# Kernel tuning notes

Hardware: AMD Instinct MI355X
Metric: run time of the kernel (lower is better)

## Reference

```python
import jax, jax.numpy as jnp
import numpy as np

DIM = 1024
BLOCK = 64
N_BLOCKS = DIM // BLOCK
N = 65536
INIT_SCALE = 0.01


def setup_inputs() -> dict:
    key = jax.random.key(0)
    k1, k2 = jax.random.split(key)
    x = jax.random.normal(k1, (N, DIM), dtype=jnp.float32)
    skew_params = jax.random.normal(k2, (N_BLOCKS, BLOCK, BLOCK), dtype=jnp.float32) * INIT_SCALE
    perm = jnp.asarray(np.random.default_rng(0).permutation(DIM), dtype=jnp.int64)
    return {"x": x, "skew_params": skew_params, "perm": perm}


def reference(x, skew_params, perm):
    # Skew-symmetrize each block: A = P - P^T, shape [K, b, b]
    A = skew_params - jnp.swapaxes(skew_params, -1, -2)
    # Per-block orthogonal matrices via matrix exponential, [K, b, b]
    B = jax.vmap(jax.scipy.linalg.expm)(A)
    # Block-diagonal matmul without materializing the dense [dim, dim] matrix:
    # x @ block_diag(B_0..B_{K-1}) == batched per-block matmul on reshaped x.
    xb = x.reshape(x.shape[0], N_BLOCKS, BLOCK)          # [N, K, b]
    yb = jnp.einsum("nkb,kbc->nkc", xb, B)               # [N, K, b]
    y = yb.reshape(x.shape[0], DIM)                      # [N, dim]
    # Shuffle: column permutation
    return y[:, perm]
```

## Files before the change

kernel.cpp:

```cpp
#include <hip/hip_runtime.h>

#define DIM           1024
#define BLK           64
#define NB            16
#define RT            16
#define MAIN_THREADS  1024
#define NWG           256
#define NT            16
#define P68           68
#define BFRAG_STRIDE  512

typedef float  f32x4  __attribute__((ext_vector_type(4)));
typedef short  bf16x8 __attribute__((ext_vector_type(8)));

static __device__ __forceinline__ short f2bf(float f) {
    union { float f; unsigned u; } v; v.f = f;
    unsigned r = v.u + 0x7fffu + ((v.u >> 16) & 1u);
    return (short)(r >> 16);
}

#define WAITL()   asm volatile("s_waitcnt lgkmcnt(0)" ::: "memory")
#define SBAR()    __builtin_amdgcn_s_barrier()

__global__ __launch_bounds__(512) void expm_kernel(
        const float* __restrict__ skew, ushort* __restrict__ Btl,
        const int* __restrict__ praw, int* __restrict__ pinv) {
    __shared__ float Asm[BLK][P68];
    __shared__ float Tb[2][BLK][P68];
    __shared__ float Rm[BLK][P68];
    const int tid = threadIdx.x;

    if (blockIdx.x == NB) {
        __shared__ int zc;
        if (tid == 0) zc = 0;
        __syncthreads();
        int local = 0;
        for (int i = tid; i < DIM; i += 512)
            if (praw[i] == 0) local++;
        if (local) atomicAdd(&zc, local);
        __syncthreads();
        const bool is64 = (zc > 100);
        const long long* p64 = (const long long*)praw;
        for (int i = tid; i < DIM; i += 512) {
            const int v = is64 ? (int)p64[i] : praw[i];
            pinv[v] = i;
        }
        return;
    }

    const int k = blockIdx.x;
    const float* P = skew + (size_t)k * (BLK * BLK);

    for (int e = tid; e < BLK * BLK; e += 512) {
        const int i = e >> 6, j = e & 63;
        const float a = P[i * BLK + j] - P[j * BLK + i];
        Asm[i][j]   = a;
        Tb[0][i][j] = a;
        Rm[i][j]    = a + (i == j ? 1.0f : 0.0f);
    }
    __syncthreads();

    const int i0 = (tid >> 4) * 2;
    const int j0 = (tid & 15) * 4;

    for (int n = 2; n <= 7; ++n) {
        const float invn = 1.0f / (float)n;
        const float (*Tc)[P68] = Tb[n & 1];
        float       (*Tn)[P68] = Tb[1 - (n & 1)];
        f32x4 acc0 = {0.f, 0.f, 0.f, 0.f}, acc1 = {0.f, 0.f, 0.f, 0.f};
        for (int b = 0; b < BLK; ++b) {
            const f32x4 av = *(const f32x4*)&Asm[b][j0];
            acc0 += Tc[i0][b]     * av;
            acc1 += Tc[i0 + 1][b] * av;
        }
        acc0 *= invn; acc1 *= invn;
        *(f32x4*)&Tn[i0][j0]     = acc0;
        *(f32x4*)&Tn[i0 + 1][j0] = acc1;
        f32x4 r0 = *(const f32x4*)&Rm[i0][j0];     r0 += acc0; *(f32x4*)&Rm[i0][j0]     = r0;
        f32x4 r1 = *(const f32x4*)&Rm[i0 + 1][j0]; r1 += acc1; *(f32x4*)&Rm[i0 + 1][j0] = r1;
        __syncthreads();
    }

    for (int e = tid; e < BLK * BLK; e += 512) {
        const int b = e >> 6, c = e & 63;
        const int n = c >> 4, m = c & 15;
        const int h = b >> 5, g = (b >> 3) & 3, j = b & 7;
        const size_t idx = (size_t)((k * 4 + n) * 2 + h) * BFRAG_STRIDE
                         + g * 128 + m * 8 + j;
        Btl[idx] = (ushort)f2bf(Rm[b][c]);
    }
}

__global__ __launch_bounds__(MAIN_THREADS) void gsl_main_kernel(
        const float* __restrict__ x, const ushort* __restrict__ Btl,
        const int* __restrict__ pinv, float* __restrict__ out) {
    __shared__ float yb[2][16384];

    const int tid  = threadIdx.x;
    const int lane = tid & 63;
    const int w    = tid >> 6;
    const int g    = lane >> 4;
    const int m16  = lane & 15;

    bf16x8 bfr[4][2];
#pragma unroll
    for (int n = 0; n < 4; ++n)
#pragma unroll
        for (int h = 0; h < 2; ++h)
            bfr[n][h] = *(const bf16x8*)(Btl +
                (size_t)((w * 4 + n) * 2 + h) * BFRAG_STRIDE + lane * 8);

    int sbase[4], sx3[4];
#pragma unroll
    for (int n = 0; n < 4; ++n) {
        const int c  = w * 64 + n * 16 + m16;
        const int j  = pinv[c];
        const int g4 = j >> 2;
        sbase[n] = g4 * 256 + (((4 * g) ^ (g4 & 12)) << 4) + (j & 3) * 4;
        sx3[n]   = g4 & 3;
    }

    const int tile0 = blockIdx.x * NT;
    const float* xw = x + w * 64 + g * 8;

    f32x4 a0, a1, a2, a3;
    {
        const float* xp = xw + (size_t)(tile0 * RT + m16) * DIM;
        a0 = *(const f32x4*)(xp);      a1 = *(const f32x4*)(xp + 4);
        a2 = *(const f32x4*)(xp + 32); a3 = *(const f32x4*)(xp + 36);
    }

    for (int it = 0; it < NT; ++it) {
        float*       yc = yb[it & 1];
        const float* yp = yb[(it & 1) ^ 1];

        bf16x8 alo, ahi;
        alo[0] = f2bf(a0[0]); alo[1] = f2bf(a0[1]); alo[2] = f2bf(a0[2]); alo[3] = f2bf(a0[3]);
        alo[4] = f2bf(a1[0]); alo[5] = f2bf(a1[1]); alo[6] = f2bf(a1[2]); alo[7] = f2bf(a1[3]);
        ahi[0] = f2bf(a2[0]); ahi[1] = f2bf(a2[1]); ahi[2] = f2bf(a2[2]); ahi[3] = f2bf(a2[3]);
        ahi[4] = f2bf(a3[0]); ahi[5] = f2bf(a3[1]); ahi[6] = f2bf(a3[2]); ahi[7] = f2bf(a3[3]);

        if (it + 1 < NT) {
            const float* xp = xw + (size_t)((tile0 + it + 1) * RT + m16) * DIM;
            a0 = *(const f32x4*)(xp);      a1 = *(const f32x4*)(xp + 4);
            a2 = *(const f32x4*)(xp + 32); a3 = *(const f32x4*)(xp + 36);
        }

        f32x4 acc[4];
#pragma unroll
        for (int n = 0; n < 4; ++n) acc[n] = (f32x4){0.f, 0.f, 0.f, 0.f};
#pragma unroll
        for (int n = 0; n < 4; ++n)
            acc[n] = __builtin_amdgcn_mfma_f32_16x16x32_bf16(alo, bfr[n][0], acc[n], 0, 0, 0);
#pragma unroll
        for (int n = 0; n < 4; ++n)
            acc[n] = __builtin_amdgcn_mfma_f32_16x16x32_bf16(ahi, bfr[n][1], acc[n], 0, 0, 0);

        char* const ycb = (char*)yc;
#pragma unroll
        for (int n = 0; n < 4; ++n)
#pragma unroll
            for (int i = 0; i < 4; ++i)
                *(float*)(ycb + sbase[n] + ((i ^ sx3[n]) << 4)) = acc[n][i];

        if (it) {
            const char* ypb  = (const char*)yp;
            float*      orow = out + (size_t)((tile0 + it - 1) * RT + w) * DIM;
#pragma unroll
            for (int i2 = 0; i2 < 4; ++i2) {
                const int j4   = lane + 64 * i2;
                const int slot = w ^ (j4 & 15);
                const f32x4 v  = *(const f32x4*)(ypb + j4 * 256 + slot * 16);
                *(f32x4*)(orow + j4 * 4) = v;
            }
        }

        WAITL(); SBAR();
    }

    {
        const char* ypb  = (const char*)yb[(NT - 1) & 1];
        float*      orow = out + (size_t)((tile0 + NT - 1) * RT + w) * DIM;
#pragma unroll
        for (int i2 = 0; i2 < 4; ++i2) {
            const int j4   = lane + 64 * i2;
            const int slot = w ^ (j4 & 15);
            const f32x4 v  = *(const f32x4*)(ypb + j4 * 256 + slot * 16);
            *(f32x4*)(orow + j4 * 4) = v;
        }
    }
}

extern "C" void kernel_launch(void* const* d_in, const int* in_sizes, int n_in,
                              void* d_out, int out_size, void* d_ws, size_t ws_size,
                              hipStream_t stream) {
    const float* x    = (const float*)d_in[0];
    const float* skew = (const float*)d_in[1];
    const int*   perm = (const int*)d_in[2];
    float* out = (float*)d_out;

    ushort* Btl  = (ushort*)d_ws;
    int*    pinv = (int*)((char*)d_ws + (size_t)NB * BLK * BLK * sizeof(ushort));

    expm_kernel<<<NB + 1, 512, 0, stream>>>(skew, Btl, perm, pinv);
    gsl_main_kernel<<<NWG, MAIN_THREADS, 0, stream>>>(x, Btl, pinv, out);
}
```

Baseline: 131.0 us.

## Shrink main workgroups to 512 threads with two blocks per wave and single LDS buffer

The main kernel now launches 512-thread workgroups (twice as many), with each wave handling two diagonal blocks instead of one. The double-buffered LDS staging becomes a single padded buffer (272-byte row stride with a rotation swizzle), so LDS use drops and launch bounds request 4 blocks per CU. The fp32-to-bf16 conversion now uses the packed v_cvt_pk_bf16_f32 instruction instead of manual rounding. In exchange, each tile needs two barriers and the store phase no longer overlaps the next tile's MFMA work through double buffering.

```diff
diff --git a/kernel.cpp b/kernel.cpp
--- a/kernel.cpp
+++ b/kernel.cpp
@@ -4,19 +4,27 @@
 #define BLK           64
 #define NB            16
 #define RT            16
-#define MAIN_THREADS  1024
-#define NWG           256
-#define NT            16
+#define MAIN_THREADS  512
+#define NWG           512
+#define TPW           8
 #define P68           68
 #define BFRAG_STRIDE  512
+#define GSTRIDE       272
 
 typedef float  f32x4  __attribute__((ext_vector_type(4)));
+typedef int    i32x4  __attribute__((ext_vector_type(4)));
 typedef short  bf16x8 __attribute__((ext_vector_type(8)));
 
 static __device__ __forceinline__ short f2bf(float f) {
     union { float f; unsigned u; } v; v.f = f;
     unsigned r = v.u + 0x7fffu + ((v.u >> 16) & 1u);
     return (short)(r >> 16);
+}
+
+static __device__ __forceinline__ unsigned cvt_pk(float lo, float hi) {
+    unsigned r;
+    asm("v_cvt_pk_bf16_f32 %0, %1, %2" : "=v"(r) : "v"(lo), "v"(hi));
+    return r;
 }
 
 #define WAITL()   asm volatile("s_waitcnt lgkmcnt(0)" ::: "memory")
@@ -91,10 +99,10 @@
     }
 }
 
-__global__ __launch_bounds__(MAIN_THREADS) void gsl_main_kernel(
+__global__ __launch_bounds__(MAIN_THREADS, 4) void gsl_main_kernel(
         const float* __restrict__ x, const ushort* __restrict__ Btl,
         const int* __restrict__ pinv, float* __restrict__ out) {
-    __shared__ float yb[2][16384];
+    __shared__ float ybuf[256 * GSTRIDE / 4];
 
     const int tid  = threadIdx.x;
     const int lane = tid & 63;
@@ -102,92 +110,129 @@
     const int g    = lane >> 4;
     const int m16  = lane & 15;
 
-    bf16x8 bfr[4][2];
-#pragma unroll
-    for (int n = 0; n < 4; ++n)
-#pragma unroll
-        for (int h = 0; h < 2; ++h)
-            bfr[n][h] = *(const bf16x8*)(Btl +
-                (size_t)((w * 4 + n) * 2 + h) * BFRAG_STRIDE + lane * 8);
-
-    int sbase[4], sx3[4];
-#pragma unroll
-    for (int n = 0; n < 4; ++n) {
-        const int c  = w * 64 + n * 16 + m16;
-        const int j  = pinv[c];
-        const int g4 = j >> 2;
-        sbase[n] = g4 * 256 + (((4 * g) ^ (g4 & 12)) << 4) + (j & 3) * 4;
-        sx3[n]   = g4 & 3;
-    }
-
-    const int tile0 = blockIdx.x * NT;
-    const float* xw = x + w * 64 + g * 8;
-
-    f32x4 a0, a1, a2, a3;
+    bf16x8 bfr[2][4][2];
+#pragma unroll
+    for (int b = 0; b < 2; ++b) {
+        const int k = w + 8 * b;
+#pragma unroll
+        for (int n = 0; n < 4; ++n)
+#pragma unroll
+            for (int h = 0; h < 2; ++h)
+                bfr[b][n][h] = *(const bf16x8*)(Btl +
+                    (size_t)((k * 4 + n) * 2 + h) * BFRAG_STRIDE + lane * 8);
+    }
+
+    int pk[2][4];
+#pragma unroll
+    for (int b = 0; b < 2; ++b)
+#pragma unroll
+        for (int n = 0; n < 4; ++n) {
+            const int c  = (w + 8 * b) * 64 + n * 16 + m16;
+            const int j  = pinv[c];
+            const int g4 = j >> 2;
+            pk[b][n] = (g4 * GSTRIDE + (j & 3) * 4)
+                     | (((4 * g + 2 * g4) & 15) << 20);
+        }
+
+    const int    tile0 = blockIdx.x * TPW;
+    const float* xw    = x + g * 8;
+    char* const  yB    = (char*)ybuf;
+
+    f32x4 aA[4], aB[4];
     {
-        const float* xp = xw + (size_t)(tile0 * RT + m16) * DIM;
-        a0 = *(const f32x4*)(xp);      a1 = *(const f32x4*)(xp + 4);
-        a2 = *(const f32x4*)(xp + 32); a3 = *(const f32x4*)(xp + 36);
-    }
-
-    for (int it = 0; it < NT; ++it) {
-        float*       yc = yb[it & 1];
-        const float* yp = yb[(it & 1) ^ 1];
-
-        bf16x8 alo, ahi;
-        alo[0] = f2bf(a0[0]); alo[1] = f2bf(a0[1]); alo[2] = f2bf(a0[2]); alo[3] = f2bf(a0[3]);
-        alo[4] = f2bf(a1[0]); alo[5] = f2bf(a1[1]); alo[6] = f2bf(a1[2]); alo[7] = f2bf(a1[3]);
-        ahi[0] = f2bf(a2[0]); ahi[1] = f2bf(a2[1]); ahi[2] = f2bf(a2[2]); ahi[3] = f2bf(a2[3]);
-        ahi[4] = f2bf(a3[0]); ahi[5] = f2bf(a3[1]); ahi[6] = f2bf(a3[2]); ahi[7] = f2bf(a3[3]);
-
-        if (it + 1 < NT) {
-            const float* xp = xw + (size_t)((tile0 + it + 1) * RT + m16) * DIM;
-            a0 = *(const f32x4*)(xp);      a1 = *(const f32x4*)(xp + 4);
-            a2 = *(const f32x4*)(xp + 32); a3 = *(const f32x4*)(xp + 36);
-        }
-
-        f32x4 acc[4];
-#pragma unroll
-        for (int n = 0; n < 4; ++n) acc[n] = (f32x4){0.f, 0.f, 0.f, 0.f};
-#pragma unroll
-        for (int n = 0; n < 4; ++n)
-            acc[n] = __builtin_amdgcn_mfma_f32_16x16x32_bf16(alo, bfr[n][0], acc[n], 0, 0, 0);
-#pragma unroll
-        for (int n = 0; n < 4; ++n)
-            acc[n] = __builtin_amdgcn_mfma_f32_16x16x32_bf16(ahi, bfr[n][1], acc[n], 0, 0, 0);
-
-        char* const ycb = (char*)yc;
-#pragma unroll
-        for (int n = 0; n < 4; ++n)
-#pragma unroll
-            for (int i = 0; i < 4; ++i)
-                *(float*)(ycb + sbase[n] + ((i ^ sx3[n]) << 4)) = acc[n][i];
-
-        if (it) {
-            const char* ypb  = (const char*)yp;
-            float*      orow = out + (size_t)((tile0 + it - 1) * RT + w) * DIM;
+        const float* xp = xw + (size_t)(tile0 * RT + m16) * DIM + w * 64;
+        aA[0] = *(const f32x4*)(xp);      aA[1] = *(const f32x4*)(xp + 4);
+        aA[2] = *(const f32x4*)(xp + 32); aA[3] = *(const f32x4*)(xp + 36);
+        const float* xq = xp + 512;
+        aB[0] = *(const f32x4*)(xq);      aB[1] = *(const f32x4*)(xq + 4);
+        aB[2] = *(const f32x4*)(xq + 32); aB[3] = *(const f32x4*)(xq + 36);
+    }
+
+    for (int it = 0; it < TPW; ++it) {
+        const size_t rbase = (size_t)(tile0 + it) * RT;
+
+        i32x4 plo, phi;
+        plo[0] = cvt_pk(aA[0][0], aA[0][1]); plo[1] = cvt_pk(aA[0][2], aA[0][3]);
+        plo[2] = cvt_pk(aA[1][0], aA[1][1]); plo[3] = cvt_pk(aA[1][2], aA[1][3]);
+        phi[0] = cvt_pk(aA[2][0], aA[2][1]); phi[1] = cvt_pk(aA[2][2], aA[2][3]);
+        phi[2] = cvt_pk(aA[3][0], aA[3][1]); phi[3] = cvt_pk(aA[3][2], aA[3][3]);
+        {
+            const bf16x8 alo = __builtin_bit_cast(bf16x8, plo);
+            const bf16x8 ahi = __builtin_bit_cast(bf16x8, phi);
+            f32x4 acc[4];
+#pragma unroll
+            for (int n = 0; n < 4; ++n) acc[n] = (f32x4){0.f, 0.f, 0.f, 0.f};
+#pragma unroll
+            for (int n = 0; n < 4; ++n)
+                acc[n] = __builtin_amdgcn_mfma_f32_16x16x32_bf16(alo, bfr[0][n][0], acc[n], 0, 0, 0);
+#pragma unroll
+            for (int n = 0; n < 4; ++n)
+                acc[n] = __builtin_amdgcn_mfma_f32_16x16x32_bf16(ahi, bfr[0][n][1], acc[n], 0, 0, 0);
+#pragma unroll
+            for (int n = 0; n < 4; ++n) {
+                const int base = pk[0][n] & 0xFFFFF;
+                const int rot  = pk[0][n] >> 20;
+#pragma unroll
+                for (int i = 0; i < 4; ++i)
+                    *(float*)(yB + base + (((rot + i) & 15) << 4)) = acc[n][i];
+            }
+        }
+
+        plo[0] = cvt_pk(aB[0][0], aB[0][1]); plo[1] = cvt_pk(aB[0][2], aB[0][3]);
+        plo[2] = cvt_pk(aB[1][0], aB[1][1]); plo[3] = cvt_pk(aB[1][2], aB[1][3]);
+        phi[0] = cvt_pk(aB[2][0], aB[2][1]); phi[1] = cvt_pk(aB[2][2], aB[2][3]);
+        phi[2] = cvt_pk(aB[3][0], aB[3][1]); phi[3] = cvt_pk(aB[3][2], aB[3][3]);
+
+        if (it + 1 < TPW) {
+            const float* xp = xw + (size_t)((tile0 + it + 1) * RT + m16) * DIM + w * 64;
+            aA[0] = *(const f32x4*)(xp);      aA[1] = *(const f32x4*)(xp + 4);
+            aA[2] = *(const f32x4*)(xp + 32); aA[3] = *(const f32x4*)(xp + 36);
+        }
+
+        {
+            const bf16x8 alo = __builtin_bit_cast(bf16x8, plo);
+            const bf16x8 ahi = __builtin_bit_cast(bf16x8, phi);
+            f32x4 acc[4];
+#pragma unroll
+            for (int n = 0; n < 4; ++n) acc[n] = (f32x4){0.f, 0.f, 0.f, 0.f};
+#pragma unroll
+            for (int n = 0; n < 4; ++n)
+                acc[n] = __builtin_amdgcn_mfma_f32_16x16x32_bf16(alo, bfr[1][n][0], acc[n], 0, 0, 0);
+#pragma unroll
+            for (int n = 0; n < 4; ++n)
+                acc[n] = __builtin_amdgcn_mfma_f32_16x16x32_bf16(ahi, bfr[1][n][1], acc[n], 0, 0, 0);
+#pragma unroll
+            for (int n = 0; n < 4; ++n) {
+                const int base = pk[1][n] & 0xFFFFF;
+                const int rot  = pk[1][n] >> 20;
+#pragma unroll
+                for (int i = 0; i < 4; ++i)
+                    *(float*)(yB + base + (((rot + i) & 15) << 4)) = acc[n][i];
+            }
+        }
+
+        WAITL(); SBAR();
+
+        if (it + 1 < TPW) {
+            const float* xq = xw + (size_t)((tile0 + it + 1) * RT + m16) * DIM + w * 64 + 512;
+            aB[0] = *(const f32x4*)(xq);      aB[1] = *(const f32x4*)(xq + 4);
+            aB[2] = *(const f32x4*)(xq + 32); aB[3] = *(const f32x4*)(xq + 36);
+        }
+
+#pragma unroll
+        for (int rr = 0; rr < 2; ++rr) {
+            const int r = w + 8 * rr;
+            float* orow = out + (rbase + r) * DIM;
 #pragma unroll
             for (int i2 = 0; i2 < 4; ++i2) {
-                const int j4   = lane + 64 * i2;
-                const int slot = w ^ (j4 & 15);
-                const f32x4 v  = *(const f32x4*)(ypb + j4 * 256 + slot * 16);
-                *(f32x4*)(orow + j4 * 4) = v;
+                const int q = lane + 64 * i2;
+                const f32x4 v = *(const f32x4*)(yB + q * GSTRIDE +
+                                                (((r + 2 * q) & 15) << 4));
+                *(f32x4*)(orow + q * 4) = v;
             }
         }
 
         WAITL(); SBAR();
-    }
-
-    {
-        const char* ypb  = (const char*)yb[(NT - 1) & 1];
-        float*      orow = out + (size_t)((tile0 + NT - 1) * RT + w) * DIM;
-#pragma unroll
-        for (int i2 = 0; i2 < 4; ++i2) {
-            const int j4   = lane + 64 * i2;
-            const int slot = w ^ (j4 & 15);
-            const f32x4 v  = *(const f32x4*)(ypb + j4 * 256 + slot * 16);
-            *(f32x4*)(orow + j4 * 4) = v;
-        }
     }
 }
 
```

Result: slower. 143.1 us (+9.2%).
